# Kernel tuning notes

Hardware: AMD Instinct MI355X
Metric: run time of the kernel (lower is better)

Reference implementation:

```python
import jax, jax.numpy as jnp
import numpy as np

B, H0, W0, C = 8, 112, 112, 192
NH, WS, SS = 6, 7, 3
HID = 4 * C


def _rel_pos_index(ws):
    coords = np.stack(np.meshgrid(np.arange(ws), np.arange(ws), indexing='ij'))  # [2,ws,ws]
    flat = coords.reshape(2, -1)
    rel = flat[:, :, None] - flat[:, None, :]          # [2,N,N]
    rel = rel.transpose(1, 2, 0).copy()                # [N,N,2]
    rel[:, :, 0] += ws - 1
    rel[:, :, 1] += ws - 1
    rel[:, :, 0] *= 2 * ws - 1
    return rel.sum(-1)                                 # [N,N]


def _attn_mask(Hp, Wp, ws, ss):
    # 0 / -100 mask for shifted windows, identical to torch get_attn_mask
    img = np.zeros((Hp, Wp))
    cnt = 0
    for hs in (slice(0, -ws), slice(-ws, -ss), slice(-ss, None)):
        for wsl in (slice(0, -ws), slice(-ws, -ss), slice(-ss, None)):
            img[hs, wsl] = cnt
            cnt += 1
    mw = img.reshape(Hp // ws, ws, Wp // ws, ws).transpose(0, 2, 1, 3).reshape(-1, ws * ws)
    am = mw[:, None, :] - mw[:, :, None]
    return np.where(am != 0, np.float32(-100.0), np.float32(0.0)).astype(np.float32)  # [nW,N,N]


def _ln(x, g, b, eps=1e-5):
    mu = jnp.mean(x, axis=-1, keepdims=True)
    var = jnp.mean(jnp.square(x - mu), axis=-1, keepdims=True)
    return (x - mu) * jax.lax.rsqrt(var + eps) * g + b


def setup_inputs() -> dict:
    key = jax.random.key(0)
    ks = jax.random.split(key, 8)
    p = lambda k, s: jax.random.normal(k, s, jnp.float32) * 0.02
    return {
        'query': jax.random.normal(ks[0], (B, H0 * W0, C), jnp.float32),
        'norm1_g': jnp.ones((C,), jnp.float32), 'norm1_b': jnp.zeros((C,), jnp.float32),
        'qkv_w': p(ks[1], (C, 3 * C)), 'qkv_b': jnp.zeros((3 * C,), jnp.float32),
        'rpb_table': p(ks[2], ((2 * WS - 1) ** 2, NH)),
        'proj_w': p(ks[3], (C, C)), 'proj_b': jnp.zeros((C,), jnp.float32),
        'norm2_g': jnp.ones((C,), jnp.float32), 'norm2_b': jnp.zeros((C,), jnp.float32),
        'fc1_w': p(ks[4], (C, HID)), 'fc1_b': jnp.zeros((HID,), jnp.float32),
        'fc2_w': p(ks[5], (HID, C)), 'fc2_b': jnp.zeros((C,), jnp.float32),
        'H': H0, 'W': W0,
    }


def reference(query, norm1_g, norm1_b, qkv_w, qkv_b, rpb_table, proj_w, proj_b,
              norm2_g, norm2_b, fc1_w, fc1_b, fc2_w, fc2_b, H, W):
    Bq, L, Cq = query.shape
    ws, ss, nh = WS, SS, NH
    hd = Cq // nh
    N = ws * ws
    # ---- W-MSA branch ----
    x = _ln(query, norm1_g, norm1_b).reshape(Bq, H, W, Cq)
    # H, W chosen divisible by ws -> pad branch is a no-op
    x = jnp.roll(x, (-ss, -ss), axis=(1, 2))            # cyclic shift
    nWh, nWw = H // ws, W // ws
    # window partition -> [B*nW, N, C]
    xw = x.reshape(Bq, nWh, ws, nWw, ws, Cq).transpose(0, 1, 3, 2, 4, 5).reshape(-1, N, Cq)
    qkv = (xw @ qkv_w + qkv_b).reshape(-1, N, 3, nh, hd).transpose(2, 0, 3, 1, 4)
    q, k, v = qkv[0] * (hd ** -0.5), qkv[1], qkv[2]     # [B_,nh,N,hd]
    attn = jnp.einsum('bhnd,bhmd->bhnm', q, k)
    bias = rpb_table[_rel_pos_index(ws).reshape(-1)].reshape(N, N, nh).transpose(2, 0, 1)
    attn = attn + bias[None]
    mask = jnp.asarray(_attn_mask(H, W, ws, ss))        # [nW,N,N]
    nW = mask.shape[0]
    attn = attn.reshape(Bq, nW, nh, N, N) + mask[None, :, None]
    attn = jax.nn.softmax(attn.reshape(-1, nh, N, N), axis=-1)
    out = jnp.einsum('bhnm,bhmd->bhnd', attn, v).transpose(0, 2, 1, 3).reshape(-1, N, Cq)
    out = out @ proj_w + proj_b
    # window reverse + reverse shift
    x = out.reshape(Bq, nWh, nWw, ws, ws, Cq).transpose(0, 1, 3, 2, 4, 5).reshape(Bq, H, W, Cq)
    x = jnp.roll(x, (ss, ss), axis=(1, 2)).reshape(Bq, H * W, Cq)
    x = query + x
    # ---- MLP branch ----
    h = _ln(x, norm2_g, norm2_b)
    h = jax.nn.gelu(h @ fc1_w + fc1_b, approximate=False)
    return x + (h @ fc2_w + fc2_b)
```

## Files before the change

kernel.cpp:

```cpp
#include <hip/hip_runtime.h>
#include <hip/hip_bf16.h>
#include <math.h>

using bf16 = __hip_bfloat16;
typedef __bf16 bf16x8 __attribute__((ext_vector_type(8)));
typedef __bf16 bf16x4 __attribute__((ext_vector_type(4)));
typedef float floatx4 __attribute__((ext_vector_type(4)));

__device__ __forceinline__ float bf2f(bf16 x) { return __bfloat162float(x); }
__device__ __forceinline__ bf16 f2bf(float x) { return __float2bfloat16(x); }

__device__ __forceinline__ float loadExt(const void* p, long i, int f32) {
  return f32 ? ((const float*)p)[i] : bf2f(((const bf16*)p)[i]);
}
__device__ __forceinline__ void storeExt(void* p, long i, int f32, float v) {
  if (f32) ((float*)p)[i] = v;
  else     ((bf16*)p)[i] = f2bf(v);
}

#define GLOAD16(gp, lp)                                                       \
  __builtin_amdgcn_global_load_lds(                                           \
      (const __attribute__((address_space(1))) void*)(gp),                    \
      (__attribute__((address_space(3))) void*)(lp), 16, 0, 0)

__global__ void detect_kernel(const unsigned int* __restrict__ q, int* __restrict__ flag) {
  const int lane = threadIdx.x;
  const unsigned int w = q[lane];
  const unsigned int lo = w & 0xffffu;
  const unsigned int e = (lo >> 7) & 0xffu;
  const bool ok = (lo == 0u) || (e >= 100u && e <= 141u);
  const unsigned long long m = __ballot(ok);
  if (lane == 0) flag[0] = (__popcll(m) == 64) ? 1 : 0;
}

__global__ void cvt_params_kernel(const int* __restrict__ flagp,
                                  const void* qkv_b, const void* proj_b,
                                  const void* n1g, const void* n1b,
                                  const void* n2g, const void* n2b,
                                  const void* fc1_b, const void* fc2_b,
                                  const void* rpb, bf16* __restrict__ dst) {
  const int f32 = (flagp[0] == 0);
  int i = blockIdx.x * blockDim.x + threadIdx.x;
  if (i >= 3510) return;
  const void* src; int j = i;
  if      (j < 576)  { src = qkv_b; }
  else if ((j -= 576)  < 192) { src = proj_b; }
  else if ((j -= 192)  < 192) { src = n1g; }
  else if ((j -= 192)  < 192) { src = n1b; }
  else if ((j -= 192)  < 192) { src = n2g; }
  else if ((j -= 192)  < 192) { src = n2b; }
  else if ((j -= 192)  < 768) { src = fc1_b; }
  else if ((j -= 768)  < 192) { src = fc2_b; }
  else { j -= 192; src = rpb; }
  dst[i] = f2bf(loadExt(src, j, f32));
}

__global__ void cvtT_kernel(const int* __restrict__ flagp, const void* __restrict__ src,
                            bf16* __restrict__ dst, int K, int N) {
  const int f32 = (flagp[0] == 0);
  int i = blockIdx.x * blockDim.x + threadIdx.x;
  if (i >= K * N) return;
  int n = i / K, k = i - n * K;
  dst[i] = f2bf(loadExt(src, (long)k * N + n, f32));
}

__global__ void biastab_kernel(const bf16* __restrict__ rpb,
                               bf16* __restrict__ btab) {
  int i = blockIdx.x * blockDim.x + threadIdx.x;
  if (i >= 6 * 2450) return;
  int head = i / 2450, r = i - head * 2450;
  int n = r / 50, m = r - n * 50;
  float v = 0.f;
  if (n < 49 && m < 49) {
    int r1 = n / 7, c1 = n - 7 * r1, r2 = m / 7, c2 = m - 7 * r2;
    v = bf2f(rpb[((r1 - r2 + 6) * 13 + (c1 - c2 + 6)) * 6 + head]);
  }
  btab[i] = f2bf(v);
}

__global__ __launch_bounds__(256) void ln_kernel(const int* __restrict__ flagp, int ext,
                                                 const void* __restrict__ x,
                                                 const bf16* __restrict__ g,
                                                 const bf16* __restrict__ b,
                                                 bf16* __restrict__ out) {
  const int f32 = ext && (flagp[0] == 0);
  const long row = (long)blockIdx.x * 4 + (threadIdx.x >> 6);
  const int lane = threadIdx.x & 63;
  const long gbase = row * 192;
  float v0 = loadExt(x, gbase + lane, f32);
  float v1 = loadExt(x, gbase + lane + 64, f32);
  float v2 = loadExt(x, gbase + lane + 128, f32);
  float s = v0 + v1 + v2;
  #pragma unroll
  for (int off = 32; off > 0; off >>= 1) s += __shfl_xor(s, off, 64);
  const float mu = s * (1.0f / 192.0f);
  float d0 = v0 - mu, d1 = v1 - mu, d2 = v2 - mu;
  float vv = d0 * d0 + d1 * d1 + d2 * d2;
  #pragma unroll
  for (int off = 32; off > 0; off >>= 1) vv += __shfl_xor(vv, off, 64);
  const float rstd = rsqrtf(vv * (1.0f / 192.0f) + 1e-5f);
  bf16* orow = out + row * 192;
  orow[lane]       = f2bf(d0 * rstd * bf2f(g[lane])       + bf2f(b[lane]));
  orow[lane + 64]  = f2bf(d1 * rstd * bf2f(g[lane + 64])  + bf2f(b[lane + 64]));
  orow[lane + 128] = f2bf(d2 * rstd * bf2f(g[lane + 128]) + bf2f(b[lane + 128]));
}

template <int EPI>
__global__ __launch_bounds__(256) void gemm_bt(const bf16* __restrict__ A,
                                               const bf16* __restrict__ BT,
                                               const bf16* __restrict__ bias,
                                               const int* __restrict__ flagp,
                                               const void* res, int res_ext,
                                               void* out, int out_ext,
                                               int M, int N, int K) {
  __shared__ __align__(16) bf16 As[3][128 * 32];
  __shared__ __align__(16) bf16 Bs[3][64 * 32];
  const int xf32 = (flagp[0] == 0);
  const int tid = threadIdx.x;
  const int wave = tid >> 6;
  const int lane = tid & 63;
  const int l16 = lane & 15;
  const int quad = lane >> 4;

  const int nbn = N >> 6;
  const int cpx = gridDim.x >> 3;
  const int wg = (gridDim.x & 7) ? (int)blockIdx.x
                                 : (blockIdx.x & 7) * cpx + (blockIdx.x >> 3);
  const int mb = wg / nbn;
  const int nb = wg - mb * nbn;
  const long m0 = (long)mb * 128;
  const int n0 = nb << 6;

  const int rS = tid >> 2;
  const int sS = tid & 3;
  const int ss = sS ^ ((rS >> 1) & 3);
  const bf16* gA0 = A + (m0 + rS) * (long)K + ss * 8;
  const bf16* gA1 = A + (m0 + rS + 64) * (long)K + ss * 8;
  const bf16* gB  = BT + (long)(n0 + rS) * K + ss * 8;

  floatx4 acc[2][4];
  #pragma unroll
  for (int i = 0; i < 2; i++)
    #pragma unroll
    for (int j = 0; j < 4; j++) acc[i][j] = (floatx4){0.f, 0.f, 0.f, 0.f};

  const int swz = (quad ^ ((l16 >> 1) & 3)) << 3;
  const int arow = wave * 32 + l16;
  const int nt = K >> 5;

  {
    GLOAD16(gA0, &As[0][tid * 8]);
    GLOAD16(gA1, &As[0][(tid + 256) * 8]);
    GLOAD16(gB,  &Bs[0][tid * 8]);
    GLOAD16(gA0 + 32, &As[1][tid * 8]);
    GLOAD16(gA1 + 32, &As[1][(tid + 256) * 8]);
    GLOAD16(gB  + 32, &Bs[1][tid * 8]);
  }

  for (int t = 0; t < nt; ++t) {
    if (t + 1 < nt) { asm volatile("s_waitcnt vmcnt(3)" ::: "memory"); }
    else            { asm volatile("s_waitcnt vmcnt(0)" ::: "memory"); }
    __builtin_amdgcn_s_barrier();
    __builtin_amdgcn_sched_barrier(0);
    if (t + 2 < nt) {
      const int p2 = (t + 2) % 3;
      const int off = (t + 2) * 32;
      GLOAD16(gA0 + off, &As[p2][tid * 8]);
      GLOAD16(gA1 + off, &As[p2][(tid + 256) * 8]);
      GLOAD16(gB  + off, &Bs[p2][tid * 8]);
    }
    const int p = t % 3;
    bf16x8 af[2], bfr[4];
    #pragma unroll
    for (int ms = 0; ms < 2; ms++)
      af[ms] = *(const bf16x8*)&As[p][(arow + ms * 16) * 32 + swz];
    #pragma unroll
    for (int ns = 0; ns < 4; ns++)
      bfr[ns] = *(const bf16x8*)&Bs[p][(ns * 16 + l16) * 32 + swz];
    #pragma unroll
    for (int ms = 0; ms < 2; ms++)
      #pragma unroll
      for (int ns = 0; ns < 4; ns++)
        acc[ms][ns] = __builtin_amdgcn_mfma_f32_16x16x32_bf16(bfr[ns], af[ms], acc[ms][ns], 0, 0, 0);
  }

  #pragma unroll
  for (int ms = 0; ms < 2; ms++) {
    const long row = m0 + wave * 32 + ms * 16 + l16;
    #pragma unroll
    for (int ns = 0; ns < 4; ns++) {
      const int col = n0 + ns * 16 + quad * 4;
      const long idx = row * (long)N + col;
      float v[4];
      #pragma unroll
      for (int r = 0; r < 4; r++) v[r] = acc[ms][ns][r] + bf2f(bias[col + r]);
      if (EPI == 1) {
        #pragma unroll
        for (int r = 0; r < 4; r++)
          v[r] = 0.5f * v[r] * (1.0f + erff(v[r] * 0.70710678118654752f));
      }
      if (EPI == 2) {
        if (res_ext && xf32) {
          const float4 t = *(const float4*)((const float*)res + idx);
          v[0] += t.x; v[1] += t.y; v[2] += t.z; v[3] += t.w;
        } else {
          const bf16x4 t = *(const bf16x4*)((const bf16*)res + idx);
          #pragma unroll
          for (int r = 0; r < 4; r++) v[r] += (float)t[r];
        }
      }
      if (out_ext && xf32) {
        float4 t; t.x = v[0]; t.y = v[1]; t.z = v[2]; t.w = v[3];
        *(float4*)((float*)out + idx) = t;
      } else {
        bf16x4 t;
        #pragma unroll
        for (int r = 0; r < 4; r++) t[r] = (__bf16)v[r];
        *(bf16x4*)((bf16*)out + idx) = t;
      }
    }
  }
}

__global__ __launch_bounds__(64, 3) void attn_kernel(const bf16* __restrict__ qkv,
                                                     const bf16* __restrict__ btab,
                                                     bf16* __restrict__ out) {
  __shared__ __align__(16) __bf16 vshT[32 * 64];
  __shared__ __align__(16) __bf16 psh[64 * 64];
  __shared__ int rowIdx[64];
  __shared__ int regn[64];
  const int lane = threadIdx.x;
  const int q = lane >> 4, l16 = lane & 15;
  const int unit = blockIdx.x;
  const int head = unit % 6;
  const int wIdx = unit / 6;
  const int b = wIdx >> 8;
  const int w2 = wIdx & 255;
  const int wh = w2 >> 4;
  const int ww = w2 & 15;

  {
    const int l = lane < 49 ? lane : 48;
    const int r = l / 7, c = l - 7 * r;
    const int hr = wh * 7 + r;
    const int wr = ww * 7 + c;
    int h = hr + 3; if (h >= 112) h -= 112;
    int w = wr + 3; if (w >= 112) w -= 112;
    rowIdx[lane] = b * 12544 + h * 112 + w;
    const int rh = hr < 105 ? 0 : (hr < 109 ? 1 : 2);
    const int rw = wr < 105 ? 0 : (wr < 109 ? 1 : 2);
    regn[lane] = (lane < 49) ? rh * 3 + rw : 99;
  }
  __syncthreads();

  int ridx[4];
  #pragma unroll
  for (int t = 0; t < 4; t++) ridx[t] = rowIdx[t * 16 + l16];

  #pragma unroll
  for (int ii = 0; ii < 4; ii++) {
    const int i = lane + ii * 64;
    const int j = i >> 2, c = (i & 3) * 8;
    const bf16x8 vv = *(const bf16x8*)&qkv[(long)rowIdx[j] * 576 + 384 + head * 32 + c];
    #pragma unroll
    for (int jj = 0; jj < 8; jj++) {
      const int d = c + jj;
      vshT[d * 64 + (((j >> 3) ^ (d & 7)) << 3) + (j & 7)] = vv[jj];
    }
  }

  floatx4 s[4][4];
  #pragma unroll
  for (int it = 0; it < 4; it++)
    #pragma unroll
    for (int jt = 0; jt < 4; jt++) s[it][jt] = (floatx4){0.f, 0.f, 0.f, 0.f};
  {
    bf16x8 afq[4], bfk[4];
    #pragma unroll
    for (int t = 0; t < 4; t++) {
      const bf16* pQ = &qkv[(long)ridx[t] * 576 + head * 32 + q * 8];
      afq[t] = *(const bf16x8*)pQ;
      bfk[t] = *(const bf16x8*)(pQ + 192);
    }
    #pragma unroll
    for (int it = 0; it < 4; it++)
      #pragma unroll
      for (int jt = 0; jt < 4; jt++)
        s[it][jt] = __builtin_amdgcn_mfma_f32_16x16x32_bf16(afq[it], bfk[jt], s[it][jt], 0, 0, 0);
  }

  int regj[4];
  #pragma unroll
  for (int jt = 0; jt < 4; jt++) regj[jt] = regn[jt * 16 + l16];
  int regi[4][4];
  #pragma unroll
  for (int it = 0; it < 4; it++)
    #pragma unroll
    for (int r = 0; r < 4; r++) regi[it][r] = regn[it * 16 + q * 4 + r];

  const bf16* bt = btab + head * 2450;
  const float scale = 0.17677669529663687f;
  float mrow[4][4];
  #pragma unroll
  for (int it = 0; it < 4; it++)
    #pragma unroll
    for (int r = 0; r < 4; r++) mrow[it][r] = -3e38f;

  #pragma unroll
  for (int it = 0; it < 4; it++)
    #pragma unroll
    for (int jt = 0; jt < 4; jt++)
      #pragma unroll
      for (int r = 0; r < 4; r++) {
        const int i = it * 16 + q * 4 + r;
        const int j = jt * 16 + l16;
        const int bi = (i < 49 ? i : 48) * 50 + (j < 49 ? j : 48);
        float v = s[it][jt][r] * scale + bf2f(bt[bi]);
        if (regi[it][r] != regj[jt]) v -= 100.0f;
        v = (j < 49) ? v : -1e30f;
        s[it][jt][r] = v;
        mrow[it][r] = fmaxf(mrow[it][r], v);
      }
  #pragma unroll
  for (int it = 0; it < 4; it++)
    #pragma unroll
    for (int r = 0; r < 4; r++) {
      float m = mrow[it][r];
      #pragma unroll
      for (int off = 1; off < 16; off <<= 1) m = fmaxf(m, __shfl_xor(m, off, 64));
      mrow[it][r] = m;
    }
  float sum[4][4];
  #pragma unroll
  for (int it = 0; it < 4; it++)
    #pragma unroll
    for (int r = 0; r < 4; r++) sum[it][r] = 0.f;
  #pragma unroll
  for (int it = 0; it < 4; it++)
    #pragma unroll
    for (int jt = 0; jt < 4; jt++)
      #pragma unroll
      for (int r = 0; r < 4; r++) {
        const float e = __expf(s[it][jt][r] - mrow[it][r]);
        s[it][jt][r] = e;
        sum[it][r] += e;
      }
  #pragma unroll
  for (int it = 0; it < 4; it++)
    #pragma unroll
    for (int r = 0; r < 4; r++) {
      float t = sum[it][r];
      #pragma unroll
      for (int off = 1; off < 16; off <<= 1) t += __shfl_xor(t, off, 64);
      mrow[it][r] = 1.0f / t;
    }

  #pragma unroll
  for (int it = 0; it < 4; it++)
    #pragma unroll
    for (int jt = 0; jt < 4; jt++)
      #pragma unroll
      for (int r = 0; r < 4; r++) {
        const int i = it * 16 + q * 4 + r;
        const int j = jt * 16 + l16;
        psh[i * 64 + (((j >> 3) ^ (i & 7)) << 3) + (j & 7)] =
            (__bf16)(s[it][jt][r] * mrow[it][r]);
      }
  __syncthreads();

  floatx4 o[4][2];
  #pragma unroll
  for (int it = 0; it < 4; it++)
    #pragma unroll
    for (int dt = 0; dt < 2; dt++) o[it][dt] = (floatx4){0.f, 0.f, 0.f, 0.f};
  #pragma unroll
  for (int ks = 0; ks < 2; ks++) {
    bf16x8 av[2];
    #pragma unroll
    for (int dt = 0; dt < 2; dt++) {
      const int row = dt * 16 + l16;
      av[dt] = *(const bf16x8*)&vshT[row * 64 + (((ks * 4 + q) ^ (row & 7)) << 3)];
    }
    #pragma unroll
    for (int it = 0; it < 4; it++) {
      const int row = it * 16 + l16;
      const bf16x8 bp = *(const bf16x8*)&psh[row * 64 + (((ks * 4 + q) ^ (row & 7)) << 3)];
      #pragma unroll
      for (int dt = 0; dt < 2; dt++)
        o[it][dt] = __builtin_amdgcn_mfma_f32_16x16x32_bf16(bp, av[dt], o[it][dt], 0, 0, 0);
    }
  }

  #pragma unroll
  for (int it = 0; it < 4; it++)
    #pragma unroll
    for (int r = 0; r < 4; r++) {
      const int i = it * 16 + q * 4 + r;
      if (i < 49) {
        const long ob = (long)rowIdx[i] * 192 + head * 32;
        #pragma unroll
        for (int dt = 0; dt < 2; dt++)
          out[ob + dt * 16 + l16] = f2bf(o[it][dt][r]);
      }
    }
}

extern "C" void kernel_launch(void* const* d_in, const int* in_sizes, int n_in,
                              void* d_out, int out_size, void* d_ws, size_t ws_size,
                              hipStream_t stream) {
  const void* query   = d_in[0];
  const void* norm1_g = d_in[1];
  const void* norm1_b = d_in[2];
  const void* qkv_w   = d_in[3];
  const void* qkv_b   = d_in[4];
  const void* rpb     = d_in[5];
  const void* proj_w  = d_in[6];
  const void* proj_b  = d_in[7];
  const void* norm2_g = d_in[8];
  const void* norm2_b = d_in[9];
  const void* fc1_w   = d_in[10];
  const void* fc1_b   = d_in[11];
  const void* fc2_w   = d_in[12];
  const void* fc2_b   = d_in[13];

  const long M = 100352;

  int* flag  = (int*)d_ws;
  bf16* base = (bf16*)((char*)d_ws + 16);
  bf16* wsA   = base;
  bf16* wsB   = wsA + M * 192;
  bf16* xbuf  = wsB + M * 768;
  bf16* qkvT  = xbuf + M * 192;
  bf16* projT = qkvT + 110592;
  bf16* fc1T  = projT + 36864;
  bf16* fc2T  = fc1T + 147456;
  bf16* pPAR  = fc2T + 147456;
  bf16* pQKVB = pPAR;
  bf16* pPRJB = pQKVB + 576;
  bf16* pN1G  = pPRJB + 192;
  bf16* pN1B  = pN1G + 192;
  bf16* pN2G  = pN1B + 192;
  bf16* pN2B  = pN2G + 192;
  bf16* pFC1B = pN2B + 192;
  bf16* pFC2B = pFC1B + 768;
  bf16* pRPB  = pFC2B + 192;
  bf16* btab  = pPAR + 3510;

  detect_kernel<<<1, 64, 0, stream>>>((const unsigned int*)query, flag);
  cvt_params_kernel<<<14, 256, 0, stream>>>(flag, qkv_b, proj_b, norm1_g, norm1_b,
                                            norm2_g, norm2_b, fc1_b, fc2_b, rpb, pPAR);
  cvtT_kernel<<<(192 * 576 + 255) / 256, 256, 0, stream>>>(flag, qkv_w, qkvT, 192, 576);
  cvtT_kernel<<<(192 * 192 + 255) / 256, 256, 0, stream>>>(flag, proj_w, projT, 192, 192);
  cvtT_kernel<<<(192 * 768 + 255) / 256, 256, 0, stream>>>(flag, fc1_w, fc1T, 192, 768);
  cvtT_kernel<<<(768 * 192 + 255) / 256, 256, 0, stream>>>(flag, fc2_w, fc2T, 768, 192);
  biastab_kernel<<<(6 * 2450 + 255) / 256, 256, 0, stream>>>(pRPB, btab);

  ln_kernel<<<M / 4, 256, 0, stream>>>(flag, 1, query, pN1G, pN1B, wsA);
  gemm_bt<0><<<784 * 9, 256, 0, stream>>>(wsA, qkvT, pQKVB, flag,
                                          nullptr, 0, wsB, 0, (int)M, 576, 192);
  attn_kernel<<<12288, 64, 0, stream>>>(wsB, btab, wsA);
  gemm_bt<2><<<784 * 3, 256, 0, stream>>>(wsA, projT, pPRJB, flag,
                                          query, 1, xbuf, 0, (int)M, 192, 192);

  ln_kernel<<<M / 4, 256, 0, stream>>>(flag, 0, xbuf, pN2G, pN2B, wsA);
  gemm_bt<1><<<784 * 12, 256, 0, stream>>>(wsA, fc1T, pFC1B, flag,
                                           nullptr, 0, wsB, 0, (int)M, 768, 192);
  gemm_bt<2><<<784 * 3, 256, 0, stream>>>(wsB, fc2T, pFC2B, flag,
                                          xbuf, 0, d_out, 1, (int)M, 192, 768);
}
```

Baseline: 615.2 us.

## Fuse LayerNorm2, FC1+GELU and FC2+residual into one MLP kernel

Replaces the LayerNorm kernel, the FC1 GEMM and the FC2 GEMM with a single kernel. Each 128-row block normalizes its rows in LDS, computes the hidden activations in 64-wide chunks with GELU, and accumulates FC2 directly, so the 768-wide hidden tensor never goes to global memory. Weight chunks are double-buffered through registers into swizzled LDS. The cost is a large LDS footprint and many accumulator registers, which limit it to one block per CU. The grid is also only 784 blocks, which may underfill the GPU.

```diff
diff --git a/kernel.cpp b/kernel.cpp
--- a/kernel.cpp
+++ b/kernel.cpp
@@ -22,6 +22,13 @@
   __builtin_amdgcn_global_load_lds(                                           \
       (const __attribute__((address_space(1))) void*)(gp),                    \
       (__attribute__((address_space(3))) void*)(lp), 16, 0, 0)
+
+#define LGKM0_BAR()                                                           \
+  do {                                                                        \
+    asm volatile("s_waitcnt lgkmcnt(0)" ::: "memory");                        \
+    __builtin_amdgcn_s_barrier();                                             \
+    __builtin_amdgcn_sched_barrier(0);                                        \
+  } while (0)
 
 __global__ void detect_kernel(const unsigned int* __restrict__ q, int* __restrict__ flag) {
   const int lane = threadIdx.x;
@@ -222,6 +229,218 @@
   }
 }
 
+__global__ __launch_bounds__(256, 1) void mlp_fused(
+    const bf16* __restrict__ xb,
+    const bf16* __restrict__ w1,
+    const bf16* __restrict__ w2,
+    const bf16* __restrict__ gN, const bf16* __restrict__ bN,
+    const bf16* __restrict__ b1, const bf16* __restrict__ b2,
+    const int* __restrict__ flagp, void* __restrict__ out) {
+  __shared__ __align__(16) __bf16 Ash[128 * 192];
+  __shared__ __align__(16) __bf16 W1sh[2][64 * 192];
+  __shared__ __align__(16) __bf16 W2sh[192 * 64];
+  __shared__ __align__(16) __bf16 Hsh[128 * 64];
+  const int xf32 = (flagp[0] == 0);
+  const int tid = threadIdx.x, wave = tid >> 6, lane = tid & 63;
+  const int l16 = lane & 15, quad = lane >> 4;
+  const int cpx = gridDim.x >> 3;
+  const int mb = (gridDim.x & 7) ? (int)blockIdx.x
+                                 : (int)(blockIdx.x & 7) * cpx + (int)(blockIdx.x >> 3);
+  const long m0 = (long)mb * 128;
+
+  {
+    const bf16* src = xb + m0 * 192;
+    #pragma unroll
+    for (int i = 0; i < 12; i++)
+      GLOAD16(src + (i * 256 + tid) * 8, &Ash[(i * 256 + tid) * 8]);
+  }
+  asm volatile("s_waitcnt vmcnt(0)" ::: "memory");
+  __builtin_amdgcn_s_barrier();
+
+  {
+    const int row = tid >> 1, half = tid & 1;
+    bf16x8 xr[12];
+    #pragma unroll
+    for (int i = 0; i < 12; i++)
+      xr[i] = *(const bf16x8*)&Ash[row * 192 + (half * 12 + i) * 8];
+    float s1 = 0.f;
+    #pragma unroll
+    for (int i = 0; i < 12; i++)
+      #pragma unroll
+      for (int j = 0; j < 8; j++) s1 += (float)xr[i][j];
+    s1 += __shfl_xor(s1, 1, 64);
+    const float mu = s1 * (1.0f / 192.0f);
+    float s2 = 0.f;
+    #pragma unroll
+    for (int i = 0; i < 12; i++)
+      #pragma unroll
+      for (int j = 0; j < 8; j++) {
+        const float d = (float)xr[i][j] - mu;
+        s2 += d * d;
+      }
+    s2 += __shfl_xor(s2, 1, 64);
+    const float rstd = rsqrtf(s2 * (1.0f / 192.0f) + 1e-5f);
+    #pragma unroll
+    for (int i = 0; i < 12; i++) {
+      const int slot = half * 12 + i;
+      const bf16x8 gg = *(const bf16x8*)&gN[slot * 8];
+      const bf16x8 bb = *(const bf16x8*)&bN[slot * 8];
+      bf16x8 nr;
+      #pragma unroll
+      for (int j = 0; j < 8; j++)
+        nr[j] = (__bf16)(((float)xr[i][j] - mu) * rstd * (float)gg[j] + (float)bb[j]);
+      xr[i] = nr;
+    }
+    __syncthreads();
+    #pragma unroll
+    for (int i = 0; i < 12; i++) {
+      const int slot = half * 12 + i;
+      const int sw = (slot & 24) | ((slot ^ row) & 7);
+      *(bf16x8*)&Ash[row * 192 + sw * 8] = xr[i];
+    }
+  }
+  __syncthreads();
+
+  bf16x8 afr[2][6];
+  #pragma unroll
+  for (int mt = 0; mt < 2; mt++)
+    #pragma unroll
+    for (int ks = 0; ks < 6; ks++) {
+      const int r = wave * 32 + mt * 16 + l16;
+      const int sl = ks * 4 + quad;
+      afr[mt][ks] = *(const bf16x8*)&Ash[r * 192 + ((sl & 24) | ((sl ^ r) & 7)) * 8];
+    }
+
+  bf16x8 st1[6], st2[6];
+  #pragma unroll
+  for (int i = 0; i < 6; i++) {
+    const int u = i * 256 + tid;
+    st1[i] = *(const bf16x8*)&w1[(u / 24) * 192 + (u % 24) * 8];
+    st2[i] = *(const bf16x8*)&w2[(u >> 3) * 768 + (u & 7) * 8];
+  }
+  #pragma unroll
+  for (int i = 0; i < 6; i++) {
+    const int u = i * 256 + tid;
+    const int r1 = u / 24, sl1 = u % 24;
+    *(bf16x8*)&W1sh[0][r1 * 192 + ((sl1 & 24) | ((sl1 ^ r1) & 7)) * 8] = st1[i];
+    const int r2 = u >> 3, sl2 = u & 7;
+    *(bf16x8*)&W2sh[r2 * 64 + ((sl2 ^ r2) & 7) * 8] = st2[i];
+  }
+  __syncthreads();
+
+  floatx4 C[12][2];
+  #pragma unroll
+  for (int nt = 0; nt < 12; nt++)
+    #pragma unroll
+    for (int mt = 0; mt < 2; mt++) C[nt][mt] = (floatx4){0.f, 0.f, 0.f, 0.f};
+
+  for (int s = 0; s < 12; ++s) {
+    const int cur = s & 1;
+    if (s + 1 < 12) {
+      #pragma unroll
+      for (int i = 0; i < 6; i++) {
+        const int u = i * 256 + tid;
+        st1[i] = *(const bf16x8*)&w1[((s + 1) * 64 + u / 24) * 192 + (u % 24) * 8];
+        st2[i] = *(const bf16x8*)&w2[(u >> 3) * 768 + (s + 1) * 64 + (u & 7) * 8];
+      }
+    }
+    floatx4 h[4][2];
+    #pragma unroll
+    for (int jt = 0; jt < 4; jt++)
+      #pragma unroll
+      for (int mt = 0; mt < 2; mt++) h[jt][mt] = (floatx4){0.f, 0.f, 0.f, 0.f};
+    #pragma unroll
+    for (int ks = 0; ks < 6; ks++) {
+      bf16x8 wf[4];
+      #pragma unroll
+      for (int jt = 0; jt < 4; jt++) {
+        const int r = jt * 16 + l16;
+        const int sl = ks * 4 + quad;
+        wf[jt] = *(const bf16x8*)&W1sh[cur][r * 192 + ((sl & 24) | ((sl ^ r) & 7)) * 8];
+      }
+      #pragma unroll
+      for (int jt = 0; jt < 4; jt++)
+        #pragma unroll
+        for (int mt = 0; mt < 2; mt++)
+          h[jt][mt] = __builtin_amdgcn_mfma_f32_16x16x32_bf16(wf[jt], afr[mt][ks], h[jt][mt], 0, 0, 0);
+    }
+    #pragma unroll
+    for (int jt = 0; jt < 4; jt++)
+      #pragma unroll
+      for (int mt = 0; mt < 2; mt++)
+        #pragma unroll
+        for (int r = 0; r < 4; r++) {
+          const int j = jt * 16 + quad * 4 + r;
+          float v = h[jt][mt][r] + bf2f(b1[s * 64 + j]);
+          v = 0.5f * v * (1.0f + erff(v * 0.70710678118654752f));
+          const int m = wave * 32 + mt * 16 + l16;
+          Hsh[m * 64 + (((jt * 2 + (quad >> 1)) ^ (l16 & 7)) & 7) * 8 + ((quad * 4 + r) & 7)] = (__bf16)v;
+        }
+    if (s + 1 < 12) {
+      #pragma unroll
+      for (int i = 0; i < 6; i++) {
+        const int u = i * 256 + tid;
+        const int r1 = u / 24, sl1 = u % 24;
+        *(bf16x8*)&W1sh[cur ^ 1][r1 * 192 + ((sl1 & 24) | ((sl1 ^ r1) & 7)) * 8] = st1[i];
+      }
+    }
+    LGKM0_BAR();
+    #pragma unroll
+    for (int k2 = 0; k2 < 2; k2++) {
+      bf16x8 hf[2];
+      #pragma unroll
+      for (int mt = 0; mt < 2; mt++) {
+        const int m = wave * 32 + mt * 16 + l16;
+        const int sl = k2 * 4 + quad;
+        hf[mt] = *(const bf16x8*)&Hsh[m * 64 + ((sl ^ (l16 & 7)) & 7) * 8];
+      }
+      #pragma unroll
+      for (int nt = 0; nt < 12; nt++) {
+        const int n = nt * 16 + l16;
+        const int sl = k2 * 4 + quad;
+        const bf16x8 wf2 = *(const bf16x8*)&W2sh[n * 64 + ((sl ^ n) & 7) * 8];
+        #pragma unroll
+        for (int mt = 0; mt < 2; mt++)
+          C[nt][mt] = __builtin_amdgcn_mfma_f32_16x16x32_bf16(wf2, hf[mt], C[nt][mt], 0, 0, 0);
+      }
+    }
+    LGKM0_BAR();
+    if (s + 1 < 12) {
+      #pragma unroll
+      for (int i = 0; i < 6; i++) {
+        const int u = i * 256 + tid;
+        const int r2 = u >> 3, sl2 = u & 7;
+        *(bf16x8*)&W2sh[r2 * 64 + ((sl2 ^ r2) & 7) * 8] = st2[i];
+      }
+    }
+  }
+
+  #pragma unroll
+  for (int mt = 0; mt < 2; mt++) {
+    const long row = m0 + wave * 32 + mt * 16 + l16;
+    #pragma unroll
+    for (int nt = 0; nt < 12; nt++) {
+      const int col = nt * 16 + quad * 4;
+      const long idx = row * 192 + col;
+      float v[4];
+      #pragma unroll
+      for (int r = 0; r < 4; r++) v[r] = C[nt][mt][r] + bf2f(b2[col + r]);
+      const bf16x4 t = *(const bf16x4*)&xb[idx];
+      #pragma unroll
+      for (int r = 0; r < 4; r++) v[r] += (float)t[r];
+      if (xf32) {
+        float4 o; o.x = v[0]; o.y = v[1]; o.z = v[2]; o.w = v[3];
+        *(float4*)((float*)out + idx) = o;
+      } else {
+        bf16x4 o;
+        #pragma unroll
+        for (int r = 0; r < 4; r++) o[r] = (__bf16)v[r];
+        *(bf16x4*)((bf16*)out + idx) = o;
+      }
+    }
+  }
+}
+
 __global__ __launch_bounds__(64, 3) void attn_kernel(const bf16* __restrict__ qkv,
                                                      const bf16* __restrict__ btab,
                                                      bf16* __restrict__ out) {
@@ -462,9 +681,6 @@
   gemm_bt<2><<<784 * 3, 256, 0, stream>>>(wsA, projT, pPRJB, flag,
                                           query, 1, xbuf, 0, (int)M, 192, 192);
 
-  ln_kernel<<<M / 4, 256, 0, stream>>>(flag, 0, xbuf, pN2G, pN2B, wsA);
-  gemm_bt<1><<<784 * 12, 256, 0, stream>>>(wsA, fc1T, pFC1B, flag,
-                                           nullptr, 0, wsB, 0, (int)M, 768, 192);
-  gemm_bt<2><<<784 * 3, 256, 0, stream>>>(wsB, fc2T, pFC2B, flag,
-                                          xbuf, 0, d_out, 1, (int)M, 192, 768);
-}
+  mlp_fused<<<784, 256, 0, stream>>>(xbuf, fc1T, fc2T, pN2G, pN2B,
+                                     pFC1B, pFC2B, flag, d_out);
+}
```

After: 652.2 us. 1.06x slower.
